# Kernel optimization log

Hardware: AMD Instinct MI355X
Metric: run time of the kernel (lower is better)

## Reference

```python
import jax, jax.numpy as jnp
import numpy as np

N_NODES = 50000
N_EDGES = 800000
IN_FEAT = 64
OUT_FEAT = 64
NUM_RELS = 200


def setup_inputs() -> dict:
    key = jax.random.key(0)
    ks = jax.random.split(key, 7)
    feat = jax.random.normal(ks[0], (N_NODES, IN_FEAT), dtype=jnp.float32)
    rel = jax.random.normal(ks[1], (NUM_RELS, IN_FEAT), dtype=jnp.float32)
    # xavier_uniform with relu gain ~ sqrt(2)*sqrt(6/(fan_in+fan_out))
    lim_wn = np.sqrt(2.0) * np.sqrt(6.0 / (4 * IN_FEAT + OUT_FEAT))
    weight_neighbor = jax.random.uniform(ks[2], (4 * IN_FEAT, OUT_FEAT), minval=-lim_wn, maxval=lim_wn, dtype=jnp.float32)
    lim_lw = np.sqrt(2.0) * np.sqrt(6.0 / (IN_FEAT + OUT_FEAT))
    loop_weight = jax.random.uniform(ks[3], (IN_FEAT, OUT_FEAT), minval=-lim_lw, maxval=lim_lw, dtype=jnp.float32)
    src = jax.random.randint(ks[4], (N_EDGES,), 0, N_NODES, dtype=jnp.int32)
    dst = jax.random.randint(ks[5], (N_EDGES,), 0, N_NODES, dtype=jnp.int32)
    etype = jax.random.randint(ks[6], (N_EDGES,), 0, NUM_RELS, dtype=jnp.int32)
    return {"feat": feat, "rel": rel, "weight_neighbor": weight_neighbor,
            "loop_weight": loop_weight, "src": src, "dst": dst, "etype": etype}


def reference(feat, rel, weight_neighbor, loop_weight, src, dst, etype):
    n = feat.shape[0]
    # edge gather
    h = feat[src]            # [E, F]
    r = rel[etype]           # [E, F]
    # message: concat([h+r, h*r, h, r]) @ W  -> [E, out]
    m = jnp.concatenate([h + r, h * r, h, r], axis=1) @ weight_neighbor
    # mean scatter-reduce to destination nodes (zero for isolated nodes, like DGL)
    s = jax.ops.segment_sum(m, dst, num_segments=n)
    cnt = jax.ops.segment_sum(jnp.ones((dst.shape[0],), feat.dtype), dst, num_segments=n)
    agg = s / jnp.maximum(cnt, 1.0)[:, None]
    # self loop (activation=None, dropout=0.0 -> identity)
    return agg + feat @ loop_weight
```

## Files before the change

### kernel.cpp

```cpp
#include <hip/hip_runtime.h>

#define F 64
#define CAP 64
#define CAPB 4608
#define EPB 8192
#define XSTR 264

typedef __attribute__((ext_vector_type(8))) short bf16x8;
typedef __attribute__((ext_vector_type(4))) float f32x4;

__device__ __forceinline__ unsigned short f2b(float x) {
    unsigned int u = __float_as_uint(x);
    return (unsigned short)((u + 0x7FFFu + ((u >> 16) & 1u)) >> 16);
}
__device__ __forceinline__ float b2f(unsigned short b) {
    return __uint_as_float(((unsigned int)b) << 16);
}

__global__ void k_pre(const float* __restrict__ wn, const float* __restrict__ lw,
                      const float* __restrict__ feat, const float* __restrict__ rel,
                      unsigned short* __restrict__ wcb, unsigned short* __restrict__ fb,
                      unsigned short* __restrict__ rb, int* __restrict__ bin_cursor,
                      int nbin, int nf4, int nr4) {
    if (blockIdx.x < 64) {
        int i = blockIdx.x * 256 + threadIdx.x;
        if (i < nbin) bin_cursor[i] = 0;
        int lane = (i >> 3) & 63, j = i & 7;
        int kt = i >> 11, nt = (i >> 9) & 3;
        int k = kt * 32 + ((lane >> 4) << 3) + j;
        int n = nt * 16 + (lane & 15);
        float v;
        if (k < 64)
            v = wn[k * 64 + n] + wn[(128 + k) * 64 + n];
        else if (k < 128)
            v = wn[(k - 64) * 64 + n] + wn[(k + 128) * 64 + n];
        else if (k < 192)
            v = wn[(k - 64) * 64 + n];
        else
            v = lw[(k - 192) * 64 + n];
        wcb[i] = f2b(v);
        return;
    }
    int c = (blockIdx.x - 64) * 256 + threadIdx.x;
    if (c < nf4) {
        float4 q = ((const float4*)feat)[c];
        ushort4 o;
        o.x = f2b(q.x); o.y = f2b(q.y); o.z = f2b(q.z); o.w = f2b(q.w);
        ((ushort4*)fb)[c] = o;
    } else if (c - nf4 < nr4) {
        int j = c - nf4;
        float4 q = ((const float4*)rel)[j];
        ushort4 o;
        o.x = f2b(q.x); o.y = f2b(q.y); o.z = f2b(q.z); o.w = f2b(q.w);
        ((ushort4*)rb)[j] = o;
    }
}

__global__ __launch_bounds__(1024) void k_bin(
    const int* __restrict__ src, const int* __restrict__ dst,
    const int* __restrict__ et, int* __restrict__ bin_cursor,
    unsigned int* __restrict__ coarse, int e) {
    __shared__ int hist[256];
    __shared__ int cur[256];

    const int t = threadIdx.x;
    if (t < 256) hist[t] = 0;
    __syncthreads();

    const int i0 = blockIdx.x * EPB + t * 8;
    int s[8], d[8], r[8];
    int nv = 0;
    if (i0 + 8 <= e) {
        int4 sa = ((const int4*)(src + i0))[0], sb = ((const int4*)(src + i0))[1];
        int4 da = ((const int4*)(dst + i0))[0], db = ((const int4*)(dst + i0))[1];
        int4 ta = ((const int4*)(et  + i0))[0], tb = ((const int4*)(et  + i0))[1];
        s[0]=sa.x; s[1]=sa.y; s[2]=sa.z; s[3]=sa.w; s[4]=sb.x; s[5]=sb.y; s[6]=sb.z; s[7]=sb.w;
        d[0]=da.x; d[1]=da.y; d[2]=da.z; d[3]=da.w; d[4]=db.x; d[5]=db.y; d[6]=db.z; d[7]=db.w;
        r[0]=ta.x; r[1]=ta.y; r[2]=ta.z; r[3]=ta.w; r[4]=tb.x; r[5]=tb.y; r[6]=tb.z; r[7]=tb.w;
        nv = 8;
    } else {
        for (int q = 0; q < 8; ++q) {
            int i = i0 + q;
            if (i < e) { s[q] = src[i]; d[q] = dst[i]; r[q] = et[i]; nv = q + 1; }
        }
    }

    for (int q = 0; q < nv; ++q) atomicAdd(&hist[d[q] >> 8], 1);
    __syncthreads();

    if (t < 256 && hist[t] > 0) cur[t] = atomicAdd(&bin_cursor[t], hist[t]);
    __syncthreads();

    for (int q = 0; q < nv; ++q) {
        int b = d[q] >> 8;
        int pos = atomicAdd(&cur[b], 1);
        if (pos < CAPB)
            coarse[b * CAPB + pos] = (unsigned int)s[q] | ((unsigned int)r[q] << 16)
                                   | ((unsigned int)(d[q] & 255) << 24);
    }
}

__global__ __launch_bounds__(1024) void k_build(
    const unsigned int* __restrict__ coarse, const int* __restrict__ bin_cursor,
    unsigned int* __restrict__ bucket, int* __restrict__ cnt, int n) {
    __shared__ int lcnt[256];
    const int t = threadIdx.x, b = blockIdx.x;
    if (t < 256) lcnt[t] = 0;
    __syncthreads();
    int ne = bin_cursor[b]; if (ne > CAPB) ne = CAPB;
    for (int i = t; i < ne; i += 1024) {
        unsigned int u = coarse[b * CAPB + i];
        int dl = (int)(u >> 24);
        int rk = atomicAdd(&lcnt[dl], 1);
        if (rk < CAP) bucket[(((b << 8) | dl) * CAP) + rk] = u & 0xFFFFFFu;
    }
    __syncthreads();
    int node = (b << 8) + t;
    if (t < 256 && node < n) cnt[node] = lcnt[t];
}

#define NPW 4

__global__ __launch_bounds__(256, 8) void k_main(
    const unsigned short* __restrict__ fb, const unsigned short* __restrict__ rb,
    const unsigned short* __restrict__ wcb, const int* __restrict__ cnt,
    const unsigned int* __restrict__ bucket,
    float* __restrict__ out, int n_nodes) {

    __shared__ unsigned short xb[16 * XSTR];

    const int lane = threadIdx.x & 63;
    const int wid  = threadIdx.x >> 6;
    const int node0 = (blockIdx.x * 4 + wid) * NPW;

#pragma unroll
    for (int n = 0; n < NPW; ++n) {
        int v = node0 + n;
        float sH = 0.f, sR = 0.f, sHR = 0.f, f0 = 0.f;
        if (v < n_nodes) {
            int deg = cnt[v];
            int m = deg < CAP ? deg : CAP;
            unsigned int pk = (lane < m) ? bucket[v * CAP + lane] : 0u;
            int j = 0;
            for (; j + 8 <= m; j += 8) {
                float h[8], r[8];
#pragma unroll
                for (int q = 0; q < 8; ++q) {
                    int u = __builtin_amdgcn_readlane((int)pk, j + q);
                    h[q] = b2f(fb[((u & 0xFFFF) << 6) + lane]);
                    r[q] = b2f(rb[(((u >> 16) & 0xFF) << 6) + lane]);
                }
#pragma unroll
                for (int q = 0; q < 8; ++q) {
                    sH += h[q]; sR += r[q]; sHR += h[q] * r[q];
                }
            }
            for (; j < m; ++j) {
                int u = __builtin_amdgcn_readlane((int)pk, j);
                float h = b2f(fb[((u & 0xFFFF) << 6) + lane]);
                float r = b2f(rb[(((u >> 16) & 0xFF) << 6) + lane]);
                sH += h; sR += r; sHR += h * r;
            }
            float inv = (deg > 0) ? 1.0f / (float)deg : 1.0f;
            sH *= inv; sR *= inv; sHR *= inv;
            f0 = b2f(fb[v * F + lane]);
        }
        unsigned short* X = &xb[(wid * NPW + n) * XSTR];
        X[lane]       = f2b(sH);
        X[64 + lane]  = f2b(sR);
        X[128 + lane] = f2b(sHR);
        X[192 + lane] = f2b(f0);
    }
    __syncthreads();

    f32x4 acc = {0.f, 0.f, 0.f, 0.f};
    const int am = lane & 15, aq = lane >> 4;
#pragma unroll
    for (int kt = 0; kt < 8; ++kt) {
        bf16x8 a = *(const bf16x8*)&xb[am * XSTR + kt * 32 + aq * 8];
        bf16x8 b = *(const bf16x8*)&wcb[(((kt * 4 + wid) * 64) + lane) * 8];
        acc = __builtin_amdgcn_mfma_f32_16x16x32_bf16(a, b, acc, 0, 0, 0);
    }

    const int colbase = wid * 16 + am;
#pragma unroll
    for (int reg = 0; reg < 4; ++reg) {
        int v = blockIdx.x * 16 + aq * 4 + reg;
        if (v < n_nodes) out[v * F + colbase] = acc[reg];
    }
}

extern "C" void kernel_launch(void* const* d_in, const int* in_sizes, int n_in,
                              void* d_out, int out_size, void* d_ws, size_t ws_size,
                              hipStream_t stream) {
    const float* feat = (const float*)d_in[0];
    const float* rel  = (const float*)d_in[1];
    const float* wn   = (const float*)d_in[2];
    const float* lw   = (const float*)d_in[3];
    const int* src = (const int*)d_in[4];
    const int* dst = (const int*)d_in[5];
    const int* et  = (const int*)d_in[6];
    float* out = (float*)d_out;

    const int N = in_sizes[0] / F;
    const int R = in_sizes[1] / F;
    const int E = in_sizes[4];
    const int nbin = (N + 255) >> 8;
    const int NF4 = N * F / 4, NR4 = R * F / 4;

    int* ws = (int*)d_ws;
    int* bin_cursor      = ws;
    int* cnt             = ws + 256;
    unsigned int* coarse = (unsigned int*)(cnt + N);
    unsigned int* bucket = coarse + (size_t)nbin * CAPB;
    unsigned short* wcb  = (unsigned short*)(bucket + (size_t)N * CAP);
    unsigned short* fb   = wcb + 16384;
    unsigned short* rb   = fb + (size_t)N * F;

    int conv_blocks = (NF4 + NR4 + 255) / 256;
    k_pre<<<64 + conv_blocks, 256, 0, stream>>>(wn, lw, feat, rel, wcb, fb, rb,
                                                bin_cursor, nbin, NF4, NR4);
    k_bin<<<(E + EPB - 1) / EPB, 1024, 0, stream>>>(src, dst, et, bin_cursor, coarse, E);
    k_build<<<nbin, 1024, 0, stream>>>(coarse, bin_cursor, bucket, cnt, N);
    int blocks = (N + 15) / 16;
    k_main<<<blocks, 256, 0, stream>>>(fb, rb, wcb, cnt, bucket, out, N);
}
```

Measured before the change: 133.6 us.

## Fuse bucket build into main kernel with per-bin flag spin-wait

Removes the separate k_build launch. The first block of each group of 16 in k_main now builds its bin's per-node buckets and counts, then publishes a flag, and the other 15 blocks spin on that flag before aggregating. This saves one kernel launch and its gap, but adds inter-block spin-waiting that depends on the builder block being scheduled before or alongside its waiters. Building with 256 threads instead of 1024 serialises more of that work.

```diff
diff --git a/kernel.cpp b/kernel.cpp
--- a/kernel.cpp
+++ b/kernel.cpp
@@ -21,10 +21,10 @@
                       const float* __restrict__ feat, const float* __restrict__ rel,
                       unsigned short* __restrict__ wcb, unsigned short* __restrict__ fb,
                       unsigned short* __restrict__ rb, int* __restrict__ bin_cursor,
-                      int nbin, int nf4, int nr4) {
+                      int* __restrict__ flag, int nf4, int nr4) {
     if (blockIdx.x < 64) {
         int i = blockIdx.x * 256 + threadIdx.x;
-        if (i < nbin) bin_cursor[i] = 0;
+        if (i < 256) { bin_cursor[i] = 0; flag[i] = 0; }
         int lane = (i >> 3) & 63, j = i & 7;
         int kt = i >> 11, nt = (i >> 9) & 3;
         int k = kt * 32 + ((lane >> 4) << 3) + j;
@@ -100,38 +100,51 @@
     }
 }
 
-__global__ __launch_bounds__(1024) void k_build(
-    const unsigned int* __restrict__ coarse, const int* __restrict__ bin_cursor,
-    unsigned int* __restrict__ bucket, int* __restrict__ cnt, int n) {
-    __shared__ int lcnt[256];
-    const int t = threadIdx.x, b = blockIdx.x;
-    if (t < 256) lcnt[t] = 0;
-    __syncthreads();
-    int ne = bin_cursor[b]; if (ne > CAPB) ne = CAPB;
-    for (int i = t; i < ne; i += 1024) {
-        unsigned int u = coarse[b * CAPB + i];
-        int dl = (int)(u >> 24);
-        int rk = atomicAdd(&lcnt[dl], 1);
-        if (rk < CAP) bucket[(((b << 8) | dl) * CAP) + rk] = u & 0xFFFFFFu;
-    }
-    __syncthreads();
-    int node = (b << 8) + t;
-    if (t < 256 && node < n) cnt[node] = lcnt[t];
-}
-
 #define NPW 4
 
 __global__ __launch_bounds__(256, 8) void k_main(
     const unsigned short* __restrict__ fb, const unsigned short* __restrict__ rb,
-    const unsigned short* __restrict__ wcb, const int* __restrict__ cnt,
-    const unsigned int* __restrict__ bucket,
+    const unsigned short* __restrict__ wcb, const unsigned int* __restrict__ coarse,
+    const int* __restrict__ bin_cursor, unsigned int* __restrict__ bucket,
+    int* __restrict__ cnt, int* __restrict__ flag,
     float* __restrict__ out, int n_nodes) {
 
     __shared__ unsigned short xb[16 * XSTR];
-
-    const int lane = threadIdx.x & 63;
-    const int wid  = threadIdx.x >> 6;
-    const int node0 = (blockIdx.x * 4 + wid) * NPW;
+    __shared__ int lcnt[256];
+
+    const int tid  = threadIdx.x;
+    const int lane = tid & 63;
+    const int wid  = tid >> 6;
+    const int bin  = blockIdx.x >> 4;
+
+    if ((blockIdx.x & 15) == 0) {
+        lcnt[tid] = 0;
+        __syncthreads();
+        int ne = bin_cursor[bin]; if (ne > CAPB) ne = CAPB;
+        for (int i = tid; i < ne; i += 256) {
+            unsigned int u = coarse[bin * CAPB + i];
+            int dl = (int)(u >> 24);
+            int rk = atomicAdd(&lcnt[dl], 1);
+            if (rk < CAP) bucket[(((bin << 8) | dl) * CAP) + rk] = u & 0xFFFFFFu;
+        }
+        __syncthreads();
+        int node = (bin << 8) + tid;
+        if (node < n_nodes) cnt[node] = lcnt[tid];
+        __syncthreads();
+        if (tid == 0) {
+            __threadfence();
+            atomicExch(&flag[bin], 1);
+        }
+    } else {
+        if (tid == 0) {
+            while (atomicAdd(&flag[bin], 0) == 0)
+                __builtin_amdgcn_s_sleep(8);
+            __threadfence();
+        }
+        __syncthreads();
+    }
+
+    const int node0 = blockIdx.x * 16 + wid * NPW;
 
 #pragma unroll
     for (int n = 0; n < NPW; ++n) {
@@ -210,7 +223,8 @@
 
     int* ws = (int*)d_ws;
     int* bin_cursor      = ws;
-    int* cnt             = ws + 256;
+    int* flag            = ws + 256;
+    int* cnt             = ws + 512;
     unsigned int* coarse = (unsigned int*)(cnt + N);
     unsigned int* bucket = coarse + (size_t)nbin * CAPB;
     unsigned short* wcb  = (unsigned short*)(bucket + (size_t)N * CAP);
@@ -219,9 +233,9 @@
 
     int conv_blocks = (NF4 + NR4 + 255) / 256;
     k_pre<<<64 + conv_blocks, 256, 0, stream>>>(wn, lw, feat, rel, wcb, fb, rb,
-                                                bin_cursor, nbin, NF4, NR4);
+                                                bin_cursor, flag, NF4, NR4);
     k_bin<<<(E + EPB - 1) / EPB, 1024, 0, stream>>>(src, dst, et, bin_cursor, coarse, E);
-    k_build<<<nbin, 1024, 0, stream>>>(coarse, bin_cursor, bucket, cnt, N);
     int blocks = (N + 15) / 16;
-    k_main<<<blocks, 256, 0, stream>>>(fb, rb, wcb, cnt, bucket, out, N);
-}
+    k_main<<<blocks, 256, 0, stream>>>(fb, rb, wcb, coarse, bin_cursor, bucket,
+                                       cnt, flag, out, N);
+}
```

After: 322.9 us. 2.42x slower.
